# Optimization experiments

Hardware: AMD Instinct MI355X
Metric: run time of the kernel (lower is better)

Reference implementation:

```python
import jax, jax.numpy as jnp
import numpy as np

B, T, V, E, H = 16, 64, 32000, 256, 1024
NEG = -1e9


def lstm_step(kernel, bias, x, h, c):
    # TF BasicLSTMCell: gates ordered i, j, f, o; forget_bias = 1.0
    z = jnp.concatenate([x, h], axis=-1) @ kernel + bias
    i, j, f, o = jnp.split(z, 4, axis=-1)
    c_new = c * jax.nn.sigmoid(f + 1.0) + jax.nn.sigmoid(i) * jnp.tanh(j)
    h_new = jnp.tanh(c_new) * jax.nn.sigmoid(o)
    return h_new, c_new


def setup_inputs() -> dict:
    key = jax.random.key(0)
    ks = jax.random.split(key, 14)
    s = 0.05
    return {
        "encoder_inputs": jax.random.randint(ks[0], (B, T), 0, V, dtype=jnp.int32),
        "decoder_inputs": jax.random.randint(ks[1], (B, T), 0, V, dtype=jnp.int32),
        "encoder_lengths": jax.random.randint(ks[2], (B,), 1, T + 1, dtype=jnp.int32),
        "decoder_lengths": jax.random.randint(ks[3], (B,), 1, T + 1, dtype=jnp.int32),
        "embedding": jax.random.uniform(ks[4], (V, E), jnp.float32, -1 / 16, 1 / 16),
        "enc_kernel": jax.random.normal(ks[5], (E + H, 4 * H), jnp.float32) * s,
        "enc_bias": jnp.zeros((4 * H,), jnp.float32),
        "dec_kernel": jax.random.normal(ks[6], (E + H + H, 4 * H), jnp.float32) * s,
        "dec_bias": jnp.zeros((4 * H,), jnp.float32),
        "Wm": jax.random.normal(ks[7], (H, H), jnp.float32) * s,
        "Wq": jax.random.normal(ks[8], (H, H), jnp.float32) * s,
        "v_att": jax.random.normal(ks[9], (H,), jnp.float32) * s,
        "attn_kernel": jax.random.normal(ks[10], (2 * H, H), jnp.float32) * s,
        "out_kernel": jax.random.normal(ks[11], (H, V), jnp.float32) * s,
    }


def _forward(encoder_inputs, decoder_inputs, encoder_lengths, decoder_lengths,
             embedding, enc_kernel, enc_bias, dec_kernel, dec_bias,
             Wm, Wq, v_att, attn_kernel, out_kernel):
    q_emb = embedding[encoder_inputs]  # [B,T,E]
    r_emb = embedding[decoder_inputs]  # [B,T,E]

    # ---- encoder: dynamic_rnn with sequence_length semantics ----
    def enc_step(carry, inp):
        h, c = carry
        x, t = inp
        h2, c2 = lstm_step(enc_kernel, enc_bias, x, h, c)
        valid = (t < encoder_lengths)[:, None]
        h = jnp.where(valid, h2, h)
        c = jnp.where(valid, c2, c)
        out = jnp.where(valid, h2, 0.0)
        return (h, c), out

    h0 = jnp.zeros((B, H), jnp.float32)
    (enc_h, enc_c), memory_tm = jax.lax.scan(
        enc_step, (h0, h0), (q_emb.transpose(1, 0, 2), jnp.arange(T)))
    memory = memory_tm.transpose(1, 0, 2)  # [B,T,H]

    keys = memory @ Wm  # precomputed Bahdanau memory projection [B,T,H]
    score_mask = jnp.arange(T)[None, :] < encoder_lengths[:, None]  # [B,T]

    # ---- decoder: AttentionWrapper(BasicLSTMCell) + TrainingHelper ----
    def dec_step(carry, inp):
        h, c, attn = carry
        x_emb, t = inp
        x = jnp.concatenate([x_emb, attn], axis=-1)  # [B, E+H]
        h2, c2 = lstm_step(dec_kernel, dec_bias, x, h, c)
        query = h2 @ Wq  # [B,H]
        scores = jnp.einsum('bth,h->bt', jnp.tanh(keys + query[:, None, :]), v_att)
        scores = jnp.where(score_mask, scores, NEG)
        align = jax.nn.softmax(scores, axis=-1)  # [B,T]
        context = jnp.einsum('bt,bth->bh', align, memory)
        attn2 = jnp.concatenate([h2, context], axis=-1) @ attn_kernel  # [B,H]
        finished = (t >= decoder_lengths)[:, None]
        out = jnp.where(finished, 0.0, attn2)  # dynamic_decode zeros finished
        return (h2, c2, attn2), out

    attn0 = jnp.zeros((B, H), jnp.float32)
    _, dec_tm = jax.lax.scan(
        dec_step, (enc_h, enc_c, attn0), (r_emb.transpose(1, 0, 2), jnp.arange(T)))
    dec_out = dec_tm.transpose(1, 0, 2)  # [B,T,H]

    logits = jnp.einsum('bth,hv->btv', dec_out, out_kernel)  # [B,T,V]
    return logits


def reference(encoder_inputs, decoder_inputs, encoder_lengths, decoder_lengths,
              embedding, enc_kernel, enc_bias, dec_kernel, dec_bias,
              Wm, Wq, v_att, attn_kernel, out_kernel):
    return _forward(encoder_inputs, decoder_inputs, encoder_lengths, decoder_lengths,
                    embedding, enc_kernel, enc_bias, dec_kernel, dec_bias,
                    Wm, Wq, v_att, attn_kernel, out_kernel)
```

## Files before the change

### kernel.cpp

```cpp
#include <hip/hip_runtime.h>
#include <hip/hip_bf16.h>

#define B_ 16
#define T_ 64
#define V_ 32000
#define E_ 256
#define H_ 1024
#define G4_ (4 * H_)
#define KE_ (E_ + H_)
#define KD_ (E_ + 2*H_)
#define NKS_ 32
#define KSE_ (KE_ / NKS_)
#define KSD_ (KD_ / NKS_)

typedef unsigned short ushort_t;
typedef unsigned int uint_t;

__device__ __forceinline__ float b2f(ushort_t u) {
    return __uint_as_float(((uint_t)u) << 16);
}
__device__ __forceinline__ ushort_t f2b(float f) {
    uint_t u = __float_as_uint(f);
    u = (u + 0x7fffu + ((u >> 16) & 1u)) >> 16;
    return (ushort_t)u;
}
__device__ __forceinline__ float sigf(float x) {
    return 1.f / (1.f + expf(-x));
}

__global__ __launch_bounds__(256) void init_kernel(float* __restrict__ p, int n)
{
    int i = blockIdx.x * 256 + threadIdx.x;
    if (i < n) p[i] = 0.f;
}

__global__ __launch_bounds__(256) void enc_gemm_kernel(
    const float* __restrict__ emb, const int* __restrict__ enc_in,
    const float* __restrict__ Wk, const float* __restrict__ h_in,
    float* __restrict__ zpart, int t)
{
    const int cc = blockIdx.x & 15;
    const int ks = blockIdx.x >> 4;
    const int col = cc * 256 + threadIdx.x;
    const int k0 = ks * KSE_;

    int vidx[16];
    #pragma unroll
    for (int b = 0; b < 16; ++b) vidx[b] = enc_in[b * T_ + t];

    float acc[16];
    #pragma unroll
    for (int b = 0; b < 16; ++b) acc[b] = 0.f;

    for (int kk = 0; kk < KSE_; ++kk) {
        const int k = k0 + kk;
        const float w = Wk[(size_t)k * G4_ + col];
        if (k < E_) {
            #pragma unroll
            for (int b = 0; b < 16; ++b)
                acc[b] = fmaf(emb[(size_t)vidx[b] * E_ + k], w, acc[b]);
        } else {
            const float* hp = h_in + (k - E_);
            #pragma unroll
            for (int b = 0; b < 16; ++b)
                acc[b] = fmaf(hp[b * H_], w, acc[b]);
        }
    }
    #pragma unroll
    for (int b = 0; b < 16; ++b)
        zpart[((size_t)(ks * 16 + b)) * G4_ + col] = acc[b];
}

__global__ __launch_bounds__(256) void enc_gates_kernel(
    const float* __restrict__ zpart, const float* __restrict__ bias,
    const int* __restrict__ enc_len, const float* __restrict__ h_in,
    float* __restrict__ h_out, float* __restrict__ c,
    float* __restrict__ memory, int t)
{
    const int idx = blockIdx.x * 256 + threadIdx.x;
    const int b = idx >> 10, hu = idx & 1023;
    float z[4];
    #pragma unroll
    for (int g = 0; g < 4; ++g) {
        float s0 = bias[g * H_ + hu], s1 = 0.f, s2 = 0.f, s3 = 0.f;
        #pragma unroll
        for (int ks = 0; ks < NKS_; ks += 4) {
            s0 += zpart[((size_t)((ks + 0) * 16 + b)) * G4_ + g * H_ + hu];
            s1 += zpart[((size_t)((ks + 1) * 16 + b)) * G4_ + g * H_ + hu];
            s2 += zpart[((size_t)((ks + 2) * 16 + b)) * G4_ + g * H_ + hu];
            s3 += zpart[((size_t)((ks + 3) * 16 + b)) * G4_ + g * H_ + hu];
        }
        z[g] = (s0 + s1) + (s2 + s3);
    }
    const float cold = c[b * H_ + hu];
    const float cn = cold * sigf(z[2] + 1.f) + sigf(z[0]) * tanhf(z[1]);
    const float hn = tanhf(cn) * sigf(z[3]);
    const bool valid = t < enc_len[b];
    h_out[b * H_ + hu] = valid ? hn : h_in[b * H_ + hu];
    c[b * H_ + hu]     = valid ? cn : cold;
    memory[((size_t)b * T_ + t) * H_ + hu] = valid ? hn : 0.f;
}

__global__ __launch_bounds__(256) void keys_gemm_kernel(
    const float* __restrict__ memory, const float* __restrict__ Wm,
    float* __restrict__ keys)
{
    const int rt = blockIdx.x >> 2;
    const int cc = blockIdx.x & 3;
    const int col = cc * 256 + threadIdx.x;
    float acc[16];
    #pragma unroll
    for (int m = 0; m < 16; ++m) acc[m] = 0.f;
    for (int k = 0; k < H_; ++k) {
        const float w = Wm[(size_t)k * H_ + col];
        const float* mp = memory + (size_t)(rt * 16) * H_ + k;
        #pragma unroll
        for (int m = 0; m < 16; ++m)
            acc[m] = fmaf(mp[(size_t)m * H_], w, acc[m]);
    }
    #pragma unroll
    for (int m = 0; m < 16; ++m)
        keys[(size_t)(rt * 16 + m) * H_ + col] = acc[m];
}

__global__ __launch_bounds__(256) void dec_gemm_kernel(
    const float* __restrict__ emb, const int* __restrict__ dec_in,
    const float* __restrict__ Wk, const float* __restrict__ attn,
    const float* __restrict__ h_in, float* __restrict__ zpart, int t)
{
    const int cc = blockIdx.x & 15;
    const int ks = blockIdx.x >> 4;
    const int col = cc * 256 + threadIdx.x;
    const int k0 = ks * KSD_;

    int vidx[16];
    #pragma unroll
    for (int b = 0; b < 16; ++b) vidx[b] = dec_in[b * T_ + t];

    float acc[16];
    #pragma unroll
    for (int b = 0; b < 16; ++b) acc[b] = 0.f;

    for (int kk = 0; kk < KSD_; ++kk) {
        const int k = k0 + kk;
        const float w = Wk[(size_t)k * G4_ + col];
        if (k < E_) {
            #pragma unroll
            for (int b = 0; b < 16; ++b)
                acc[b] = fmaf(emb[(size_t)vidx[b] * E_ + k], w, acc[b]);
        } else if (k < E_ + H_) {
            const float* ap = attn + (k - E_);
            #pragma unroll
            for (int b = 0; b < 16; ++b)
                acc[b] = fmaf(ap[b * H_], w, acc[b]);
        } else {
            const float* hp = h_in + (k - E_ - H_);
            #pragma unroll
            for (int b = 0; b < 16; ++b)
                acc[b] = fmaf(hp[b * H_], w, acc[b]);
        }
    }
    #pragma unroll
    for (int b = 0; b < 16; ++b)
        zpart[((size_t)(ks * 16 + b)) * G4_ + col] = acc[b];
}

__global__ __launch_bounds__(256) void dec_gates_kernel(
    const float* __restrict__ zpart, const float* __restrict__ bias,
    float* __restrict__ h_out, float* __restrict__ c)
{
    const int idx = blockIdx.x * 256 + threadIdx.x;
    const int b = idx >> 10, hu = idx & 1023;
    float z[4];
    #pragma unroll
    for (int g = 0; g < 4; ++g) {
        float s0 = bias[g * H_ + hu], s1 = 0.f, s2 = 0.f, s3 = 0.f;
        #pragma unroll
        for (int ks = 0; ks < NKS_; ks += 4) {
            s0 += zpart[((size_t)((ks + 0) * 16 + b)) * G4_ + g * H_ + hu];
            s1 += zpart[((size_t)((ks + 1) * 16 + b)) * G4_ + g * H_ + hu];
            s2 += zpart[((size_t)((ks + 2) * 16 + b)) * G4_ + g * H_ + hu];
            s3 += zpart[((size_t)((ks + 3) * 16 + b)) * G4_ + g * H_ + hu];
        }
        z[g] = (s0 + s1) + (s2 + s3);
    }
    const float cold = c[b * H_ + hu];
    const float cn = cold * sigf(z[2] + 1.f) + sigf(z[0]) * tanhf(z[1]);
    const float hn = tanhf(cn) * sigf(z[3]);
    h_out[b * H_ + hu] = hn;
    c[b * H_ + hu] = cn;
}

__global__ __launch_bounds__(256) void query_gemm_kernel(
    const float* __restrict__ h2, const float* __restrict__ Wq,
    float* __restrict__ qpart)
{
    const int cc = blockIdx.x & 3;
    const int ks = blockIdx.x >> 2;
    const int col = cc * 256 + threadIdx.x;
    const int k0 = ks * 32;
    float acc[16];
    #pragma unroll
    for (int b = 0; b < 16; ++b) acc[b] = 0.f;
    for (int kk = 0; kk < 32; ++kk) {
        const int k = k0 + kk;
        const float w = Wq[(size_t)k * H_ + col];
        const float* hp = h2 + k;
        #pragma unroll
        for (int b = 0; b < 16; ++b)
            acc[b] = fmaf(hp[b * H_], w, acc[b]);
    }
    #pragma unroll
    for (int b = 0; b < 16; ++b)
        qpart[((size_t)(ks * 16 + b)) * H_ + col] = acc[b];
}

__global__ __launch_bounds__(256) void query_finish_kernel(
    const float* __restrict__ qpart, float* __restrict__ q)
{
    const int idx = blockIdx.x * 256 + threadIdx.x;
    const int b = idx >> 10, col = idx & 1023;
    float s0 = 0.f, s1 = 0.f, s2 = 0.f, s3 = 0.f;
    #pragma unroll
    for (int ks = 0; ks < 32; ks += 4) {
        s0 += qpart[((size_t)((ks + 0) * 16 + b)) * H_ + col];
        s1 += qpart[((size_t)((ks + 1) * 16 + b)) * H_ + col];
        s2 += qpart[((size_t)((ks + 2) * 16 + b)) * H_ + col];
        s3 += qpart[((size_t)((ks + 3) * 16 + b)) * H_ + col];
    }
    q[idx] = (s0 + s1) + (s2 + s3);
}

__global__ __launch_bounds__(256) void attn_scores_kernel(
    const float* __restrict__ q, const float* __restrict__ keys,
    const float* __restrict__ v_att, float* __restrict__ scores)
{
    const int b = blockIdx.x >> 6, t = blockIdx.x & 63;
    const int tid = threadIdx.x;
    const float* kp = keys + ((size_t)b * T_ + t) * H_;
    const float* qp = q + b * H_;
    float s = 0.f;
    #pragma unroll
    for (int i = 0; i < 4; ++i) {
        const int h = tid + i * 256;
        s += tanhf(kp[h] + qp[h]) * v_att[h];
    }
    #pragma unroll
    for (int off = 32; off; off >>= 1) s += __shfl_xor(s, off);
    __shared__ float red[4];
    if ((tid & 63) == 0) red[tid >> 6] = s;
    __syncthreads();
    if (tid == 0) scores[b * T_ + t] = (red[0] + red[1]) + (red[2] + red[3]);
}

__global__ __launch_bounds__(256) void softmax_ctx_kernel(
    const float* __restrict__ scores, const float* __restrict__ memory,
    const int* __restrict__ enc_len, float* __restrict__ ctx)
{
    const int b = blockIdx.x >> 2, cc = blockIdx.x & 3;
    const int tid = threadIdx.x;
    __shared__ float al[T_];
    if (tid < 64) {
        const int len = enc_len[b];
        float s = (tid < len) ? scores[b * T_ + tid] : -1e9f;
        float m = s;
        #pragma unroll
        for (int off = 32; off; off >>= 1) m = fmaxf(m, __shfl_xor(m, off));
        float e = expf(s - m);
        float sum = e;
        #pragma unroll
        for (int off = 32; off; off >>= 1) sum += __shfl_xor(sum, off);
        al[tid] = e / sum;
    }
    __syncthreads();
    const int col = cc * 256 + tid;
    const float* mp = memory + (size_t)b * T_ * H_ + col;
    float a0 = 0.f, a1 = 0.f, a2 = 0.f, a3 = 0.f;
    #pragma unroll
    for (int t2 = 0; t2 < T_; t2 += 4) {
        a0 = fmaf(al[t2 + 0], mp[(size_t)(t2 + 0) * H_], a0);
        a1 = fmaf(al[t2 + 1], mp[(size_t)(t2 + 1) * H_], a1);
        a2 = fmaf(al[t2 + 2], mp[(size_t)(t2 + 2) * H_], a2);
        a3 = fmaf(al[t2 + 3], mp[(size_t)(t2 + 3) * H_], a3);
    }
    ctx[b * H_ + col] = (a0 + a1) + (a2 + a3);
}

__global__ __launch_bounds__(256) void attnout_gemm_kernel(
    const float* __restrict__ h2, const float* __restrict__ ctx,
    const float* __restrict__ attn_k, float* __restrict__ apart)
{
    const int cc = blockIdx.x & 3;
    const int ks = blockIdx.x >> 2;
    const int col = cc * 256 + threadIdx.x;
    const int k0 = ks * 64;
    float acc[16];
    #pragma unroll
    for (int b = 0; b < 16; ++b) acc[b] = 0.f;
    for (int kk = 0; kk < 64; ++kk) {
        const int k = k0 + kk;
        const float w = attn_k[(size_t)k * H_ + col];
        const float* xp = (k < H_) ? (h2 + k) : (ctx + (k - H_));
        #pragma unroll
        for (int b = 0; b < 16; ++b)
            acc[b] = fmaf(xp[b * H_], w, acc[b]);
    }
    #pragma unroll
    for (int b = 0; b < 16; ++b)
        apart[((size_t)(ks * 16 + b)) * H_ + col] = acc[b];
}

__global__ __launch_bounds__(256) void attnout_finish_kernel(
    const float* __restrict__ apart, const int* __restrict__ dec_len,
    float* __restrict__ attn_state, float* __restrict__ dec_out, int t)
{
    const int idx = blockIdx.x * 256 + threadIdx.x;
    const int b = idx >> 10, col = idx & 1023;
    float s0 = 0.f, s1 = 0.f, s2 = 0.f, s3 = 0.f;
    #pragma unroll
    for (int ks = 0; ks < 32; ks += 4) {
        s0 += apart[((size_t)((ks + 0) * 16 + b)) * H_ + col];
        s1 += apart[((size_t)((ks + 1) * 16 + b)) * H_ + col];
        s2 += apart[((size_t)((ks + 2) * 16 + b)) * H_ + col];
        s3 += apart[((size_t)((ks + 3) * 16 + b)) * H_ + col];
    }
    const float s = (s0 + s1) + (s2 + s3);
    attn_state[b * H_ + col] = s;
    const bool fin = t >= dec_len[b];
    dec_out[((size_t)b * T_ + t) * H_ + col] = fin ? 0.f : s;
}

typedef __attribute__((ext_vector_type(8))) short short8;
typedef __attribute__((ext_vector_type(4))) float float4v;

__global__ __launch_bounds__(256) void logits_kernel(
    const float* __restrict__ A, const float* __restrict__ Bw,
    float* __restrict__ out)
{
    __shared__ __align__(16) ushort_t Ah[64][40];
    __shared__ __align__(16) ushort_t Al[64][40];
    __shared__ __align__(16) ushort_t Bh[64][40];
    __shared__ __align__(16) ushort_t Bl[64][40];
    const int tid = threadIdx.x;
    const int m0 = blockIdx.x * 64;
    const int n0 = blockIdx.y * 64;
    const int wv = tid >> 6, lane = tid & 63;
    const int ml = lane & 15, quad = lane >> 4;

    float4v acc[4];
    #pragma unroll
    for (int nn = 0; nn < 4; ++nn) acc[nn] = (float4v){0.f, 0.f, 0.f, 0.f};

    for (int kb = 0; kb < 1024; kb += 32) {
        __syncthreads();
        {
            const int r = tid >> 2, c0 = (tid & 3) * 8;
            const float* ap = A + (size_t)(m0 + r) * 1024 + kb + c0;
            #pragma unroll
            for (int i = 0; i < 8; ++i) {
                const float f = ap[i];
                const ushort_t hi = f2b(f);
                Ah[r][c0 + i] = hi;
                Al[r][c0 + i] = f2b(f - b2f(hi));
            }
        }
        {
            const int cB = tid & 63, kq = tid >> 6;
            #pragma unroll
            for (int i = 0; i < 8; ++i) {
                const int k = kq * 8 + i;
                const float f = Bw[(size_t)(kb + k) * V_ + n0 + cB];
                const ushort_t hi = f2b(f);
                Bh[cB][k] = hi;
                Bl[cB][k] = f2b(f - b2f(hi));
            }
        }
        __syncthreads();
        const short8 afh = *(const short8*)&Ah[wv * 16 + ml][quad * 8];
        const short8 afl = *(const short8*)&Al[wv * 16 + ml][quad * 8];
        #pragma unroll
        for (int nn = 0; nn < 4; ++nn) {
            const short8 bfh = *(const short8*)&Bh[nn * 16 + ml][quad * 8];
            const short8 bfl = *(const short8*)&Bl[nn * 16 + ml][quad * 8];
            acc[nn] = __builtin_amdgcn_mfma_f32_16x16x32_bf16(afh, bfh, acc[nn], 0, 0, 0);
            acc[nn] = __builtin_amdgcn_mfma_f32_16x16x32_bf16(afh, bfl, acc[nn], 0, 0, 0);
            acc[nn] = __builtin_amdgcn_mfma_f32_16x16x32_bf16(afl, bfh, acc[nn], 0, 0, 0);
        }
    }
    #pragma unroll
    for (int nn = 0; nn < 4; ++nn) {
        #pragma unroll
        for (int rg = 0; rg < 4; ++rg) {
            const int row = m0 + wv * 16 + quad * 4 + rg;
            const int colo = n0 + nn * 16 + ml;
            out[(size_t)row * V_ + colo] = acc[nn][rg];
        }
    }
}

extern "C" void kernel_launch(void* const* d_in, const int* in_sizes, int n_in,
                              void* d_out, int out_size, void* d_ws, size_t ws_size,
                              hipStream_t stream) {
    (void)in_sizes; (void)n_in; (void)out_size; (void)ws_size;
    const int*   enc_in  = (const int*)d_in[0];
    const int*   dec_in  = (const int*)d_in[1];
    const int*   enc_len = (const int*)d_in[2];
    const int*   dec_len = (const int*)d_in[3];
    const float* emb     = (const float*)d_in[4];
    const float* encK    = (const float*)d_in[5];
    const float* encB    = (const float*)d_in[6];
    const float* decK    = (const float*)d_in[7];
    const float* decB    = (const float*)d_in[8];
    const float* Wm      = (const float*)d_in[9];
    const float* Wq      = (const float*)d_in[10];
    const float* v_att   = (const float*)d_in[11];
    const float* attnK   = (const float*)d_in[12];
    const float* outK    = (const float*)d_in[13];
    float* out = (float*)d_out;

    float* hbuf    = (float*)d_ws;
    float* cbuf    = hbuf + 2 * B_ * H_;
    float* attn    = cbuf + B_ * H_;
    float* ctx     = attn + B_ * H_;
    float* q       = ctx + B_ * H_;
    float* scores  = q + B_ * H_;
    float* memory  = scores + B_ * T_;
    float* keys    = memory + (size_t)B_ * T_ * H_;
    float* dec_out = keys + (size_t)B_ * T_ * H_;
    float* zpart   = dec_out + (size_t)B_ * T_ * H_;
    float* qpart   = zpart;
    float* apart   = zpart + (size_t)32 * B_ * H_;

    const int ninit = 4 * B_ * H_;
    init_kernel<<<(ninit + 255) / 256, 256, 0, stream>>>((float*)d_ws, ninit);

    for (int t = 0; t < T_; ++t) {
        float* h_in  = hbuf + (t & 1) * B_ * H_;
        float* h_out = hbuf + ((t + 1) & 1) * B_ * H_;
        enc_gemm_kernel<<<512, 256, 0, stream>>>(emb, enc_in, encK, h_in, zpart, t);
        enc_gates_kernel<<<64, 256, 0, stream>>>(zpart, encB, enc_len, h_in,
                                                 h_out, cbuf, memory, t);
    }
    keys_gemm_kernel<<<256, 256, 0, stream>>>(memory, Wm, keys);

    for (int t = 0; t < T_; ++t) {
        float* h_in  = hbuf + (t & 1) * B_ * H_;
        float* h2    = hbuf + ((t + 1) & 1) * B_ * H_;
        dec_gemm_kernel<<<512, 256, 0, stream>>>(emb, dec_in, decK, attn, h_in, zpart, t);
        dec_gates_kernel<<<64, 256, 0, stream>>>(zpart, decB, h2, cbuf);
        query_gemm_kernel<<<128, 256, 0, stream>>>(h2, Wq, qpart);
        query_finish_kernel<<<64, 256, 0, stream>>>(qpart, q);
        attn_scores_kernel<<<1024, 256, 0, stream>>>(q, keys, v_att, scores);
        softmax_ctx_kernel<<<64, 256, 0, stream>>>(scores, memory, enc_len, ctx);
        attnout_gemm_kernel<<<128, 256, 0, stream>>>(h2, ctx, attnK, apart);
        attnout_finish_kernel<<<64, 256, 0, stream>>>(apart, dec_len, attn, dec_out, t);
    }

    logits_kernel<<<dim3(16, 500), 256, 0, stream>>>(dec_out, outK, out);
}
```

Before: 7.006 ms.

## Vectorize recurrent GEMMs, fuse attention kernels, pre-split logits operands to bf16

The encoder, decoder, keys and attention-output GEMMs now read activations as float4 and unroll k by four. The split-K query GEMM and its finish kernel become a single per-batch q kernel, and the score and softmax-context kernels merge into one block per batch. Together these cut per-timestep launches in the decoder loop. The logits path pre-splits the output kernel into transposed bf16 hi/lo arrays and the activations into hi/lo, then runs an MFMA kernel that reads directly from global memory. This costs extra workspace and a separate conversion pass over a large weight matrix.

```diff
diff --git a/kernel.cpp b/kernel.cpp
--- a/kernel.cpp
+++ b/kernel.cpp
@@ -1,5 +1,4 @@
 #include <hip/hip_runtime.h>
-#include <hip/hip_bf16.h>
 
 #define B_ 16
 #define T_ 64
@@ -15,6 +14,8 @@
 
 typedef unsigned short ushort_t;
 typedef unsigned int uint_t;
+typedef __attribute__((ext_vector_type(8))) short short8;
+typedef __attribute__((ext_vector_type(4))) float float4v;
 
 __device__ __forceinline__ float b2f(ushort_t u) {
     return __uint_as_float(((uint_t)u) << 16);
@@ -28,6 +29,7 @@
     return 1.f / (1.f + expf(-x));
 }
 
+
 __global__ __launch_bounds__(256) void init_kernel(float* __restrict__ p, int n)
 {
     int i = blockIdx.x * 256 + threadIdx.x;
@@ -52,18 +54,32 @@
     #pragma unroll
     for (int b = 0; b < 16; ++b) acc[b] = 0.f;
 
-    for (int kk = 0; kk < KSE_; ++kk) {
-        const int k = k0 + kk;
-        const float w = Wk[(size_t)k * G4_ + col];
+    for (int g = 0; g < KSE_ / 4; ++g) {
+        const int k = k0 + g * 4;
+        const float* wp = Wk + (size_t)k * G4_ + col;
+        const float w0 = wp[0];
+        const float w1 = wp[G4_];
+        const float w2 = wp[2 * G4_];
+        const float w3 = wp[3 * G4_];
         if (k < E_) {
             #pragma unroll
-            for (int b = 0; b < 16; ++b)
-                acc[b] = fmaf(emb[(size_t)vidx[b] * E_ + k], w, acc[b]);
+            for (int b = 0; b < 16; ++b) {
+                const float4 xv = *(const float4*)(emb + (size_t)vidx[b] * E_ + k);
+                acc[b] = fmaf(xv.x, w0, acc[b]);
+                acc[b] = fmaf(xv.y, w1, acc[b]);
+                acc[b] = fmaf(xv.z, w2, acc[b]);
+                acc[b] = fmaf(xv.w, w3, acc[b]);
+            }
         } else {
             const float* hp = h_in + (k - E_);
             #pragma unroll
-            for (int b = 0; b < 16; ++b)
-                acc[b] = fmaf(hp[b * H_], w, acc[b]);
+            for (int b = 0; b < 16; ++b) {
+                const float4 xv = *(const float4*)(hp + b * H_);
+                acc[b] = fmaf(xv.x, w0, acc[b]);
+                acc[b] = fmaf(xv.y, w1, acc[b]);
+                acc[b] = fmaf(xv.z, w2, acc[b]);
+                acc[b] = fmaf(xv.w, w3, acc[b]);
+            }
         }
     }
     #pragma unroll
@@ -111,12 +127,19 @@
     float acc[16];
     #pragma unroll
     for (int m = 0; m < 16; ++m) acc[m] = 0.f;
-    for (int k = 0; k < H_; ++k) {
-        const float w = Wm[(size_t)k * H_ + col];
+    for (int g = 0; g < H_ / 4; ++g) {
+        const int k = g * 4;
+        const float* wp = Wm + (size_t)k * H_ + col;
+        const float w0 = wp[0], w1 = wp[H_], w2 = wp[2 * H_], w3 = wp[3 * H_];
         const float* mp = memory + (size_t)(rt * 16) * H_ + k;
         #pragma unroll
-        for (int m = 0; m < 16; ++m)
-            acc[m] = fmaf(mp[(size_t)m * H_], w, acc[m]);
+        for (int m = 0; m < 16; ++m) {
+            const float4 xv = *(const float4*)(mp + (size_t)m * H_);
+            acc[m] = fmaf(xv.x, w0, acc[m]);
+            acc[m] = fmaf(xv.y, w1, acc[m]);
+            acc[m] = fmaf(xv.z, w2, acc[m]);
+            acc[m] = fmaf(xv.w, w3, acc[m]);
+        }
     }
     #pragma unroll
     for (int m = 0; m < 16; ++m)
@@ -141,23 +164,33 @@
     #pragma unroll
     for (int b = 0; b < 16; ++b) acc[b] = 0.f;
 
-    for (int kk = 0; kk < KSD_; ++kk) {
-        const int k = k0 + kk;
-        const float w = Wk[(size_t)k * G4_ + col];
+    for (int g = 0; g < KSD_ / 4; ++g) {
+        const int k = k0 + g * 4;
+        const float* wp = Wk + (size_t)k * G4_ + col;
+        const float w0 = wp[0];
+        const float w1 = wp[G4_];
+        const float w2 = wp[2 * G4_];
+        const float w3 = wp[3 * G4_];
         if (k < E_) {
             #pragma unroll
-            for (int b = 0; b < 16; ++b)
-                acc[b] = fmaf(emb[(size_t)vidx[b] * E_ + k], w, acc[b]);
-        } else if (k < E_ + H_) {
-            const float* ap = attn + (k - E_);
-            #pragma unroll
-            for (int b = 0; b < 16; ++b)
-                acc[b] = fmaf(ap[b * H_], w, acc[b]);
+            for (int b = 0; b < 16; ++b) {
+                const float4 xv = *(const float4*)(emb + (size_t)vidx[b] * E_ + k);
+                acc[b] = fmaf(xv.x, w0, acc[b]);
+                acc[b] = fmaf(xv.y, w1, acc[b]);
+                acc[b] = fmaf(xv.z, w2, acc[b]);
+                acc[b] = fmaf(xv.w, w3, acc[b]);
+            }
         } else {
-            const float* hp = h_in + (k - E_ - H_);
-            #pragma unroll
-            for (int b = 0; b < 16; ++b)
-                acc[b] = fmaf(hp[b * H_], w, acc[b]);
+            const float* xb = (k < E_ + H_) ? (attn + (k - E_))
+                                            : (h_in + (k - E_ - H_));
+            #pragma unroll
+            for (int b = 0; b < 16; ++b) {
+                const float4 xv = *(const float4*)(xb + b * H_);
+                acc[b] = fmaf(xv.x, w0, acc[b]);
+                acc[b] = fmaf(xv.y, w1, acc[b]);
+                acc[b] = fmaf(xv.z, w2, acc[b]);
+                acc[b] = fmaf(xv.w, w3, acc[b]);
+            }
         }
     }
     #pragma unroll
@@ -191,99 +224,77 @@
     c[b * H_ + hu] = cn;
 }
 
-__global__ __launch_bounds__(256) void query_gemm_kernel(
+__global__ __launch_bounds__(256) void q_kernel(
     const float* __restrict__ h2, const float* __restrict__ Wq,
-    float* __restrict__ qpart)
-{
-    const int cc = blockIdx.x & 3;
-    const int ks = blockIdx.x >> 2;
+    float* __restrict__ q)
+{
+    const int b = blockIdx.x >> 2, cc = blockIdx.x & 3;
     const int col = cc * 256 + threadIdx.x;
-    const int k0 = ks * 32;
-    float acc[16];
-    #pragma unroll
-    for (int b = 0; b < 16; ++b) acc[b] = 0.f;
-    for (int kk = 0; kk < 32; ++kk) {
-        const int k = k0 + kk;
-        const float w = Wq[(size_t)k * H_ + col];
-        const float* hp = h2 + k;
-        #pragma unroll
-        for (int b = 0; b < 16; ++b)
-            acc[b] = fmaf(hp[b * H_], w, acc[b]);
-    }
-    #pragma unroll
-    for (int b = 0; b < 16; ++b)
-        qpart[((size_t)(ks * 16 + b)) * H_ + col] = acc[b];
-}
-
-__global__ __launch_bounds__(256) void query_finish_kernel(
-    const float* __restrict__ qpart, float* __restrict__ q)
-{
-    const int idx = blockIdx.x * 256 + threadIdx.x;
-    const int b = idx >> 10, col = idx & 1023;
-    float s0 = 0.f, s1 = 0.f, s2 = 0.f, s3 = 0.f;
-    #pragma unroll
-    for (int ks = 0; ks < 32; ks += 4) {
-        s0 += qpart[((size_t)((ks + 0) * 16 + b)) * H_ + col];
-        s1 += qpart[((size_t)((ks + 1) * 16 + b)) * H_ + col];
-        s2 += qpart[((size_t)((ks + 2) * 16 + b)) * H_ + col];
-        s3 += qpart[((size_t)((ks + 3) * 16 + b)) * H_ + col];
-    }
-    q[idx] = (s0 + s1) + (s2 + s3);
-}
-
-__global__ __launch_bounds__(256) void attn_scores_kernel(
+    const float* hp = h2 + b * H_;
+    float acc = 0.f;
+    for (int g = 0; g < H_ / 4; ++g) {
+        const int k = g * 4;
+        const float* wp = Wq + (size_t)k * H_ + col;
+        const float4 xv = *(const float4*)(hp + k);
+        acc = fmaf(xv.x, wp[0], acc);
+        acc = fmaf(xv.y, wp[H_], acc);
+        acc = fmaf(xv.z, wp[2 * H_], acc);
+        acc = fmaf(xv.w, wp[3 * H_], acc);
+    }
+    q[b * H_ + col] = acc;
+}
+
+__global__ __launch_bounds__(256) void sc_ctx_kernel(
     const float* __restrict__ q, const float* __restrict__ keys,
-    const float* __restrict__ v_att, float* __restrict__ scores)
-{
-    const int b = blockIdx.x >> 6, t = blockIdx.x & 63;
+    const float* __restrict__ v_att, const float* __restrict__ memory,
+    const int* __restrict__ enc_len, float* __restrict__ ctx)
+{
+    const int b = blockIdx.x;
     const int tid = threadIdx.x;
-    const float* kp = keys + ((size_t)b * T_ + t) * H_;
+    const int wv = tid >> 6, lane = tid & 63;
+    __shared__ float sc[T_];
+    __shared__ float al[T_];
     const float* qp = q + b * H_;
-    float s = 0.f;
-    #pragma unroll
-    for (int i = 0; i < 4; ++i) {
-        const int h = tid + i * 256;
-        s += tanhf(kp[h] + qp[h]) * v_att[h];
-    }
-    #pragma unroll
-    for (int off = 32; off; off >>= 1) s += __shfl_xor(s, off);
-    __shared__ float red[4];
-    if ((tid & 63) == 0) red[tid >> 6] = s;
+    for (int tt = wv; tt < T_; tt += 4) {
+        const float* kp = keys + ((size_t)b * T_ + tt) * H_;
+        float s = 0.f;
+        #pragma unroll
+        for (int j = 0; j < 16; ++j) {
+            const int h = lane + j * 64;
+            s += tanhf(kp[h] + qp[h]) * v_att[h];
+        }
+        #pragma unroll
+        for (int off = 32; off; off >>= 1) s += __shfl_xor(s, off);
+        if (lane == 0) sc[tt] = s;
+    }
     __syncthreads();
-    if (tid == 0) scores[b * T_ + t] = (red[0] + red[1]) + (red[2] + red[3]);
-}
-
-__global__ __launch_bounds__(256) void softmax_ctx_kernel(
-    const float* __restrict__ scores, const float* __restrict__ memory,
-    const int* __restrict__ enc_len, float* __restrict__ ctx)
-{
-    const int b = blockIdx.x >> 2, cc = blockIdx.x & 3;
-    const int tid = threadIdx.x;
-    __shared__ float al[T_];
     if (tid < 64) {
         const int len = enc_len[b];
-        float s = (tid < len) ? scores[b * T_ + tid] : -1e9f;
+        float s = (tid < len) ? sc[tid] : -1e9f;
         float m = s;
         #pragma unroll
         for (int off = 32; off; off >>= 1) m = fmaxf(m, __shfl_xor(m, off));
-        float e = expf(s - m);
+        const float e = expf(s - m);
         float sum = e;
         #pragma unroll
         for (int off = 32; off; off >>= 1) sum += __shfl_xor(sum, off);
         al[tid] = e / sum;
     }
     __syncthreads();
-    const int col = cc * 256 + tid;
-    const float* mp = memory + (size_t)b * T_ * H_ + col;
-    float a0 = 0.f, a1 = 0.f, a2 = 0.f, a3 = 0.f;
-    #pragma unroll
-    for (int t2 = 0; t2 < T_; t2 += 4) {
-        a0 = fmaf(al[t2 + 0], mp[(size_t)(t2 + 0) * H_], a0);
-        a1 = fmaf(al[t2 + 1], mp[(size_t)(t2 + 1) * H_], a1);
-        a2 = fmaf(al[t2 + 2], mp[(size_t)(t2 + 2) * H_], a2);
-        a3 = fmaf(al[t2 + 3], mp[(size_t)(t2 + 3) * H_], a3);
-    }
-    ctx[b * H_ + col] = (a0 + a1) + (a2 + a3);
+    #pragma unroll
+    for (int i = 0; i < 4; ++i) {
+        const int col = tid + i * 256;
+        const float* mp = memory + (size_t)b * T_ * H_ + col;
+        float a0 = 0.f, a1 = 0.f, a2 = 0.f, a3 = 0.f;
+        #pragma unroll
+        for (int t2 = 0; t2 < T_; t2 += 4) {
+            a0 = fmaf(al[t2 + 0], mp[(size_t)(t2 + 0) * H_], a0);
+            a1 = fmaf(al[t2 + 1], mp[(size_t)(t2 + 1) * H_], a1);
+            a2 = fmaf(al[t2 + 2], mp[(size_t)(t2 + 2) * H_], a2);
+            a3 = fmaf(al[t2 + 3], mp[(size_t)(t2 + 3) * H_], a3);
+        }
+        ctx[b * H_ + col] = (a0 + a1) + (a2 + a3);
+    }
 }
 
 __global__ __launch_bounds__(256) void attnout_gemm_kernel(
@@ -297,13 +308,20 @@
     float acc[16];
     #pragma unroll
     for (int b = 0; b < 16; ++b) acc[b] = 0.f;
-    for (int kk = 0; kk < 64; ++kk) {
-        const int k = k0 + kk;
-        const float w = attn_k[(size_t)k * H_ + col];
-        const float* xp = (k < H_) ? (h2 + k) : (ctx + (k - H_));
-        #pragma unroll
-        for (int b = 0; b < 16; ++b)
-            acc[b] = fmaf(xp[b * H_], w, acc[b]);
+    #pragma unroll
+    for (int g = 0; g < 16; ++g) {
+        const int k = k0 + g * 4;
+        const float* wp = attn_k + (size_t)k * H_ + col;
+        const float w0 = wp[0], w1 = wp[H_], w2 = wp[2 * H_], w3 = wp[3 * H_];
+        const float* xb = (k < H_) ? (h2 + k) : (ctx + (k - H_));
+        #pragma unroll
+        for (int b = 0; b < 16; ++b) {
+            const float4 xv = *(const float4*)(xb + b * H_);
+            acc[b] = fmaf(xv.x, w0, acc[b]);
+            acc[b] = fmaf(xv.y, w1, acc[b]);
+            acc[b] = fmaf(xv.z, w2, acc[b]);
+            acc[b] = fmaf(xv.w, w3, acc[b]);
+        }
     }
     #pragma unroll
     for (int b = 0; b < 16; ++b)
@@ -330,17 +348,125 @@
     dec_out[((size_t)b * T_ + t) * H_ + col] = fin ? 0.f : s;
 }
 
-typedef __attribute__((ext_vector_type(8))) short short8;
-typedef __attribute__((ext_vector_type(4))) float float4v;
+__global__ __launch_bounds__(256) void bsplit_kernel(
+    const float* __restrict__ Bw, ushort_t* __restrict__ Bh_t,
+    ushort_t* __restrict__ Bl_t)
+{
+    __shared__ ushort_t Th[64][65];
+    __shared__ ushort_t Tl[64][65];
+    const int k0 = (blockIdx.x & 15) * 64;
+    const int n0 = (blockIdx.x >> 4) * 64;
+    const int tid = threadIdx.x;
+    {
+        const int nl = tid & 63, kb = tid >> 6;
+        for (int i = 0; i < 16; ++i) {
+            const int kl = kb + i * 4;
+            const float f = Bw[(size_t)(k0 + kl) * V_ + n0 + nl];
+            const ushort_t hi = f2b(f);
+            Th[kl][nl] = hi;
+            Tl[kl][nl] = f2b(f - b2f(hi));
+        }
+    }
+    __syncthreads();
+    {
+        const int r = tid >> 2, c0 = (tid & 3) * 16;
+        short8 vh0, vh1, vl0, vl1;
+        #pragma unroll
+        for (int j = 0; j < 8; ++j) {
+            vh0[j] = (short)Th[c0 + j][r];
+            vh1[j] = (short)Th[c0 + 8 + j][r];
+            vl0[j] = (short)Tl[c0 + j][r];
+            vl1[j] = (short)Tl[c0 + 8 + j][r];
+        }
+        ushort_t* ph = Bh_t + (size_t)(n0 + r) * 1024 + k0 + c0;
+        ushort_t* pl = Bl_t + (size_t)(n0 + r) * 1024 + k0 + c0;
+        *(short8*)ph = vh0;
+        *(short8*)(ph + 8) = vh1;
+        *(short8*)pl = vl0;
+        *(short8*)(pl + 8) = vl1;
+    }
+}
+
+__global__ __launch_bounds__(256) void asplit_kernel(
+    const float* __restrict__ A, ushort_t* __restrict__ Ah_g,
+    ushort_t* __restrict__ Al_g)
+{
+    const size_t i0 = ((size_t)blockIdx.x * 256 + threadIdx.x) * 8;
+    const float4 f0 = *(const float4*)(A + i0);
+    const float4 f1 = *(const float4*)(A + i0 + 4);
+    float f[8] = {f0.x, f0.y, f0.z, f0.w, f1.x, f1.y, f1.z, f1.w};
+    short8 vh, vl;
+    #pragma unroll
+    for (int j = 0; j < 8; ++j) {
+        const ushort_t hi = f2b(f[j]);
+        vh[j] = (short)hi;
+        vl[j] = (short)f2b(f[j] - b2f(hi));
+    }
+    *(short8*)(Ah_g + i0) = vh;
+    *(short8*)(Al_g + i0) = vl;
+}
+
+__global__ __launch_bounds__(256) void logits_pre_kernel(
+    const ushort_t* __restrict__ Ah_g, const ushort_t* __restrict__ Al_g,
+    const ushort_t* __restrict__ Bh_t, const ushort_t* __restrict__ Bl_t,
+    float* __restrict__ out)
+{
+    const int tid = threadIdx.x;
+    const int m0 = blockIdx.x * 128;
+    const int n0 = blockIdx.y * 64;
+    const int w = tid >> 6, lane = tid & 63;
+    const int ml = lane & 15, quad = lane >> 4;
+
+    float4v acc[2][4];
+    #pragma unroll
+    for (int ms = 0; ms < 2; ++ms)
+        #pragma unroll
+        for (int nn = 0; nn < 4; ++nn) acc[ms][nn] = (float4v){0.f, 0.f, 0.f, 0.f};
+
+    const size_t arow0 = (size_t)(m0 + w * 32 + ml) * 1024;
+    const size_t arow1 = (size_t)(m0 + w * 32 + 16 + ml) * 1024;
+
+    for (int kb = 0; kb < 1024; kb += 32) {
+        const int ko = kb + quad * 8;
+        const short8 ah0 = *(const short8*)(Ah_g + arow0 + ko);
+        const short8 al0 = *(const short8*)(Al_g + arow0 + ko);
+        const short8 ah1 = *(const short8*)(Ah_g + arow1 + ko);
+        const short8 al1 = *(const short8*)(Al_g + arow1 + ko);
+        #pragma unroll
+        for (int nn = 0; nn < 4; ++nn) {
+            const size_t brow = (size_t)(n0 + nn * 16 + ml) * 1024 + ko;
+            const short8 bfh = *(const short8*)(Bh_t + brow);
+            const short8 bfl = *(const short8*)(Bl_t + brow);
+            acc[0][nn] = __builtin_amdgcn_mfma_f32_16x16x32_bf16(ah0, bfh, acc[0][nn], 0, 0, 0);
+            acc[0][nn] = __builtin_amdgcn_mfma_f32_16x16x32_bf16(ah0, bfl, acc[0][nn], 0, 0, 0);
+            acc[0][nn] = __builtin_amdgcn_mfma_f32_16x16x32_bf16(al0, bfh, acc[0][nn], 0, 0, 0);
+            acc[1][nn] = __builtin_amdgcn_mfma_f32_16x16x32_bf16(ah1, bfh, acc[1][nn], 0, 0, 0);
+            acc[1][nn] = __builtin_amdgcn_mfma_f32_16x16x32_bf16(ah1, bfl, acc[1][nn], 0, 0, 0);
+            acc[1][nn] = __builtin_amdgcn_mfma_f32_16x16x32_bf16(al1, bfh, acc[1][nn], 0, 0, 0);
+        }
+    }
+    #pragma unroll
+    for (int ms = 0; ms < 2; ++ms) {
+        #pragma unroll
+        for (int nn = 0; nn < 4; ++nn) {
+            #pragma unroll
+            for (int rg = 0; rg < 4; ++rg) {
+                const int row = m0 + w * 32 + ms * 16 + quad * 4 + rg;
+                const int colo = n0 + nn * 16 + ml;
+                out[(size_t)row * V_ + colo] = acc[ms][nn][rg];
+            }
+        }
+    }
+}
 
 __global__ __launch_bounds__(256) void logits_kernel(
     const float* __restrict__ A, const float* __restrict__ Bw,
     float* __restrict__ out)
 {
-    __shared__ __align__(16) ushort_t Ah[64][40];
-    __shared__ __align__(16) ushort_t Al[64][40];
-    __shared__ __align__(16) ushort_t Bh[64][40];
-    __shared__ __align__(16) ushort_t Bl[64][40];
+    __shared__ __align__(16) ushort_t Ah[64][44];
+    __shared__ __align__(16) ushort_t Al[64][44];
+    __shared__ __align__(16) ushort_t Bh[64][44];
+    __shared__ __align__(16) ushort_t Bl[64][44];
     const int tid = threadIdx.x;
     const int m0 = blockIdx.x * 64;
     const int n0 = blockIdx.y * 64;
@@ -401,7 +527,7 @@
 extern "C" void kernel_launch(void* const* d_in, const int* in_sizes, int n_in,
                               void* d_out, int out_size, void* d_ws, size_t ws_size,
                               hipStream_t stream) {
-    (void)in_sizes; (void)n_in; (void)out_size; (void)ws_size;
+    (void)in_sizes; (void)n_in; (void)out_size;
     const int*   enc_in  = (const int*)d_in[0];
     const int*   dec_in  = (const int*)d_in[1];
     const int*   enc_len = (const int*)d_in[2];
@@ -428,11 +554,21 @@
     float* keys    = memory + (size_t)B_ * T_ * H_;
     float* dec_out = keys + (size_t)B_ * T_ * H_;
     float* zpart   = dec_out + (size_t)B_ * T_ * H_;
-    float* qpart   = zpart;
-    float* apart   = zpart + (size_t)32 * B_ * H_;
+    float* apart   = zpart;
+    float* base_end = zpart + (size_t)NKS_ * B_ * G4_;
+
+    ushort_t* Ah_g = (ushort_t*)base_end;
+    ushort_t* Al_g = Ah_g + (size_t)1024 * 1024;
+    ushort_t* Bh_t = Al_g + (size_t)1024 * 1024;
+    ushort_t* Bl_t = Bh_t + (size_t)V_ * 1024;
+    const size_t need = 21368832ull + 2ull * 2097152ull + 2ull * 65536000ull;
+    const bool use_pre = ws_size >= need;
 
     const int ninit = 4 * B_ * H_;
     init_kernel<<<(ninit + 255) / 256, 256, 0, stream>>>((float*)d_ws, ninit);
+
+    if (use_pre)
+        bsplit_kernel<<<16 * 500, 256, 0, stream>>>(outK, Bh_t, Bl_t);
 
     for (int t = 0; t < T_; ++t) {
         float* h_in  = hbuf + (t & 1) * B_ * H_;
@@ -444,17 +580,20 @@
     keys_gemm_kernel<<<256, 256, 0, stream>>>(memory, Wm, keys);
 
     for (int t = 0; t < T_; ++t) {
-        float* h_in  = hbuf + (t & 1) * B_ * H_;
-        float* h2    = hbuf + ((t + 1) & 1) * B_ * H_;
+        float* h_in = hbuf + (t & 1) * B_ * H_;
+        float* h2   = hbuf + ((t + 1) & 1) * B_ * H_;
         dec_gemm_kernel<<<512, 256, 0, stream>>>(emb, dec_in, decK, attn, h_in, zpart, t);
         dec_gates_kernel<<<64, 256, 0, stream>>>(zpart, decB, h2, cbuf);
-        query_gemm_kernel<<<128, 256, 0, stream>>>(h2, Wq, qpart);
-        query_finish_kernel<<<64, 256, 0, stream>>>(qpart, q);
-        attn_scores_kernel<<<1024, 256, 0, stream>>>(q, keys, v_att, scores);
-        softmax_ctx_kernel<<<64, 256, 0, stream>>>(scores, memory, enc_len, ctx);
+        q_kernel<<<64, 256, 0, stream>>>(h2, Wq, q);
+        sc_ctx_kernel<<<16, 256, 0, stream>>>(q, keys, v_att, memory, enc_len, ctx);
         attnout_gemm_kernel<<<128, 256, 0, stream>>>(h2, ctx, attnK, apart);
         attnout_finish_kernel<<<64, 256, 0, stream>>>(apart, dec_len, attn, dec_out, t);
     }
 
-    logits_kernel<<<dim3(16, 500), 256, 0, stream>>>(dec_out, outK, out);
-}
+    if (use_pre) {
+        asplit_kernel<<<512, 256, 0, stream>>>(dec_out, Ah_g, Al_g);
+        logits_pre_kernel<<<dim3(8, 500), 256, 0, stream>>>(Ah_g, Al_g, Bh_t, Bl_t, out);
+    } else {
+        logits_kernel<<<dim3(16, 500), 256, 0, stream>>>(dec_out, outK, out);
+    }
+}
```

Measured after the change: 16.02 ms. 129% more time.
